# Kernel tuning notes

Hardware: AMD Instinct MI355X
Metric: run time of the kernel (lower is better)

The kernel has to match this reference:

```python
import jax, jax.numpy as jnp
import numpy as np

D_MODEL = 32
SEQ = 128  # input_dim: each scalar feature is a token


def setup_inputs() -> dict:
    key = jax.random.key(0)
    ks = jax.random.split(key, 11)
    B = 16384
    s = 1.0 / np.sqrt(D_MODEL)
    return {
        "x": jax.random.normal(ks[0], (B, SEQ), dtype=jnp.float32),
        "Wt": jax.random.normal(ks[1], (1, D_MODEL), dtype=jnp.float32),  # token_proj weight (in=1)
        "bt": jax.random.normal(ks[2], (D_MODEL,), dtype=jnp.float32) * 0.02,
        "Wq": jax.random.normal(ks[3], (D_MODEL, D_MODEL), dtype=jnp.float32) * s,
        "bq": jax.random.normal(ks[4], (D_MODEL,), dtype=jnp.float32) * 0.02,
        "Wk": jax.random.normal(ks[5], (D_MODEL, D_MODEL), dtype=jnp.float32) * s,
        "bk": jax.random.normal(ks[6], (D_MODEL,), dtype=jnp.float32) * 0.02,
        "Wv": jax.random.normal(ks[7], (D_MODEL, D_MODEL), dtype=jnp.float32) * s,
        "bv": jax.random.normal(ks[8], (D_MODEL,), dtype=jnp.float32) * 0.02,
        "Wo": jax.random.normal(ks[9], (D_MODEL, 1), dtype=jnp.float32) * s,
        "bo": jax.random.normal(ks[10], (1,), dtype=jnp.float32) * 0.02,
    }


def reference(x, Wt, bt, Wq, bq, Wk, bk, Wv, bv, Wo, bo):
    # x: [B, 128] -> tokens [B, 128, d_model] (each scalar projected from 1 -> d)
    tokens = x[..., None] * Wt[0] + bt  # [B, S, D]
    Q = jnp.einsum("bsd,de->bse", tokens, Wq) + bq
    K = jnp.einsum("bsd,de->bse", tokens, Wk) + bk
    V = jnp.einsum("bsd,de->bse", tokens, Wv) + bv
    scale = jnp.asarray(D_MODEL, x.dtype) ** 0.5
    scores = jnp.einsum("bqd,bkd->bqk", Q, K) / scale  # [B, S, S]
    w = jax.nn.softmax(scores, axis=-1)
    att = jnp.einsum("bqk,bkd->bqd", w, V)  # [B, S, D]
    agg = att.mean(axis=1)  # [B, D]
    risk = agg @ Wo + bo  # [B, 1]
    return risk[:, 0]
```

## Files before the change

### kernel.cpp

```cpp
#include <hip/hip_runtime.h>
#include <hip/hip_bf16.h>

#define SEQ 128
#define DM 32

#define K_LOG2E_2P23 12102203.161561485f
#define SCHRAUDOLPH_C 1064985472.0f

__global__ void precompute_consts(const float* __restrict__ Wt,
                                  const float* __restrict__ bt,
                                  const float* __restrict__ Wq,
                                  const float* __restrict__ bq,
                                  const float* __restrict__ Wk,
                                  const float* __restrict__ bk,
                                  const float* __restrict__ Wv,
                                  const float* __restrict__ bv,
                                  const float* __restrict__ Wo,
                                  const float* __restrict__ bo,
                                  float* __restrict__ consts) {
    int e = threadIdx.x;
    float qw = 0.f, qb = 0.f, kw = 0.f, kb = 0.f, vw = 0.f, vb = 0.f;
    float wo = 0.f;
    if (e < DM) {
        for (int d = 0; d < DM; ++d) {
            float wt = Wt[d];
            float bb = bt[d];
            qw = fmaf(wt, Wq[d * DM + e], qw);
            qb = fmaf(bb, Wq[d * DM + e], qb);
            kw = fmaf(wt, Wk[d * DM + e], kw);
            kb = fmaf(bb, Wk[d * DM + e], kb);
            vw = fmaf(wt, Wv[d * DM + e], vw);
            vb = fmaf(bb, Wv[d * DM + e], vb);
        }
        qb += bq[e];
        kb += bk[e];
        vb += bv[e];
        wo = Wo[e];
    }
    float pa = qw * kw;
    float pc = qb * kw;
    float pal = vw * wo;
    float pbe = vb * wo;
    for (int off = 32; off > 0; off >>= 1) {
        pa  += __shfl_down(pa, off);
        pc  += __shfl_down(pc, off);
        pal += __shfl_down(pal, off);
        pbe += __shfl_down(pbe, off);
    }
    if (e == 0) {
        const float inv_scale = 0.17677669529663687f;
        consts[0] = pa * inv_scale * K_LOG2E_2P23;
        consts[1] = pc * inv_scale * K_LOG2E_2P23;
        consts[2] = pal;
        consts[3] = pbe + bo[0];
    }
}

template <bool CLAMP>
__device__ __forceinline__ void row_loop(const float4* __restrict__ row4,
                                         float T0, float M0, float T1, float M1,
                                         float& s0, float& sxw0,
                                         float& s1, float& sxw1) {
#pragma unroll
    for (int k4 = 0; k4 < SEQ / 4; ++k4) {
        const float4 xv = row4[k4];
#pragma unroll
        for (int j = 0; j < 4; ++j) {
            const float xk = (j == 0) ? xv.x : (j == 1) ? xv.y : (j == 2) ? xv.z : xv.w;
            float v0 = fmaf(T0, xk, M0);
            float v1 = fmaf(T1, xk, M1);
            if (CLAMP) {
                v0 = fmaxf(v0, 0.0f);
                v1 = fmaxf(v1, 0.0f);
            }
            const float e0 = __int_as_float((int)v0);
            const float e1 = __int_as_float((int)v1);
            s0 += e0; sxw0 = fmaf(e0, xk, sxw0);
            s1 += e1; sxw1 = fmaf(e1, xk, sxw1);
        }
    }
}

#define ROWS_PER_BLOCK 4

__global__ __launch_bounds__(256) void attn_rowmean_kernel(
        const float* __restrict__ x,
        const float* __restrict__ consts,
        float* __restrict__ out, int B) {
    __shared__ float sx[ROWS_PER_BLOCK][SEQ];

    const int wave = threadIdx.x >> 6;
    const int lane = threadIdx.x & 63;
    int b = blockIdx.x * ROWS_PER_BLOCK + wave;
    if (b >= B) b = B - 1;

    const float A     = consts[0];
    const float C     = consts[1];
    const float alpha = consts[2];
    const float beta  = consts[3];

    const float* xr = x + (size_t)b * SEQ;
    const float x0 = xr[lane];
    const float x1 = xr[lane + 64];
    sx[wave][lane]      = x0;
    sx[wave][lane + 64] = x1;

    float mx = fmaxf(x0, x1);
    float mn = fminf(x0, x1);
    for (int off = 32; off > 0; off >>= 1) {
        mx = fmaxf(mx, __shfl_xor(mx, off));
        mn = fminf(mn, __shfl_xor(mn, off));
    }

    __syncthreads();

    const float T0 = fmaf(A, x0, C);
    const float T1 = fmaf(A, x1, C);
    const float m0 = fmaxf(T0 * mx, T0 * mn);
    const float m1 = fmaxf(T1 * mx, T1 * mn);
    const float M0 = SCHRAUDOLPH_C - m0;
    const float M1 = SCHRAUDOLPH_C - m1;

    float s0 = 0.f, sxw0 = 0.f, s1 = 0.f, sxw1 = 0.f;
    const float4* row4 = (const float4*)sx[wave];

    const float maxabs = fmaxf(fabsf(mx), fabsf(mn));
    const float tmax = fmaf(fabsf(A), maxabs, fabsf(C));
    if (tmax * (mx - mn) < 1.0e9f) {
        row_loop<false>(row4, T0, M0, T1, M1, s0, sxw0, s1, sxw1);
    } else {
        row_loop<true>(row4, T0, M0, T1, M1, s0, sxw0, s1, sxw1);
    }

    float msum = sxw0 * __builtin_amdgcn_rcpf(s0) +
                 sxw1 * __builtin_amdgcn_rcpf(s1);
    for (int off = 32; off > 0; off >>= 1)
        msum += __shfl_xor(msum, off);

    if (lane == 0)
        out[b] = fmaf(alpha, msum * (1.0f / 128.0f), beta);
}

extern "C" void kernel_launch(void* const* d_in, const int* in_sizes, int n_in,
                              void* d_out, int out_size, void* d_ws, size_t ws_size,
                              hipStream_t stream) {
    const float* x  = (const float*)d_in[0];
    const float* Wt = (const float*)d_in[1];
    const float* bt = (const float*)d_in[2];
    const float* Wq = (const float*)d_in[3];
    const float* bq = (const float*)d_in[4];
    const float* Wk = (const float*)d_in[5];
    const float* bk = (const float*)d_in[6];
    const float* Wv = (const float*)d_in[7];
    const float* bv = (const float*)d_in[8];
    const float* Wo = (const float*)d_in[9];
    const float* bo = (const float*)d_in[10];
    float* out = (float*)d_out;
    float* consts = (float*)d_ws;

    const int B = in_sizes[0] / SEQ;

    precompute_consts<<<1, 64, 0, stream>>>(Wt, bt, Wq, bq, Wk, bk, Wv, bv,
                                            Wo, bo, consts);

    const int grid = (B + ROWS_PER_BLOCK - 1) / ROWS_PER_BLOCK;
    attn_rowmean_kernel<<<grid, 256, 0, stream>>>(x, consts, out, B);
}
```

Before: 98.40 us.

## Fuse constant precompute into main kernel and process two rows per wave

Removes the separate single-block precompute launch. Each wave now recomputes the folded attention constants (A, C, alpha, beta) from the weight matrices itself and then handles two batch rows instead of one. This saves one kernel launch and the serialising dependency between the two kernels. In exchange every wave repeats about 16 iterations of weight loads and FMAs plus shuffle reductions, and the __syncthreads is dropped because each wave reads only its own shared-memory rows.

```diff
diff --git a/kernel.cpp b/kernel.cpp
--- a/kernel.cpp
+++ b/kernel.cpp
@@ -6,55 +6,8 @@
 
 #define K_LOG2E_2P23 12102203.161561485f
 #define SCHRAUDOLPH_C 1064985472.0f
+#define INV_SQRT_D 0.17677669529663687f
 
-__global__ void precompute_consts(const float* __restrict__ Wt,
-                                  const float* __restrict__ bt,
-                                  const float* __restrict__ Wq,
-                                  const float* __restrict__ bq,
-                                  const float* __restrict__ Wk,
-                                  const float* __restrict__ bk,
-                                  const float* __restrict__ Wv,
-                                  const float* __restrict__ bv,
-                                  const float* __restrict__ Wo,
-                                  const float* __restrict__ bo,
-                                  float* __restrict__ consts) {
-    int e = threadIdx.x;
-    float qw = 0.f, qb = 0.f, kw = 0.f, kb = 0.f, vw = 0.f, vb = 0.f;
-    float wo = 0.f;
-    if (e < DM) {
-        for (int d = 0; d < DM; ++d) {
-            float wt = Wt[d];
-            float bb = bt[d];
-            qw = fmaf(wt, Wq[d * DM + e], qw);
-            qb = fmaf(bb, Wq[d * DM + e], qb);
-            kw = fmaf(wt, Wk[d * DM + e], kw);
-            kb = fmaf(bb, Wk[d * DM + e], kb);
-            vw = fmaf(wt, Wv[d * DM + e], vw);
-            vb = fmaf(bb, Wv[d * DM + e], vb);
-        }
-        qb += bq[e];
-        kb += bk[e];
-        vb += bv[e];
-        wo = Wo[e];
-    }
-    float pa = qw * kw;
-    float pc = qb * kw;
-    float pal = vw * wo;
-    float pbe = vb * wo;
-    for (int off = 32; off > 0; off >>= 1) {
-        pa  += __shfl_down(pa, off);
-        pc  += __shfl_down(pc, off);
-        pal += __shfl_down(pal, off);
-        pbe += __shfl_down(pbe, off);
-    }
-    if (e == 0) {
-        const float inv_scale = 0.17677669529663687f;
-        consts[0] = pa * inv_scale * K_LOG2E_2P23;
-        consts[1] = pc * inv_scale * K_LOG2E_2P23;
-        consts[2] = pal;
-        consts[3] = pbe + bo[0];
-    }
-}
 
 template <bool CLAMP>
 __device__ __forceinline__ void row_loop(const float4* __restrict__ row4,
@@ -81,64 +34,116 @@
     }
 }
 
-#define ROWS_PER_BLOCK 4
+#define WAVES_PER_BLOCK 4
+#define ROWS_PER_WAVE 2
 
-__global__ __launch_bounds__(256) void attn_rowmean_kernel(
+__global__ __launch_bounds__(256) void attn_fused_kernel(
         const float* __restrict__ x,
-        const float* __restrict__ consts,
+        const float* __restrict__ Wt, const float* __restrict__ bt,
+        const float* __restrict__ Wq, const float* __restrict__ bq,
+        const float* __restrict__ Wk,
+        const float* __restrict__ Wv, const float* __restrict__ bv,
+        const float* __restrict__ Wo, const float* __restrict__ bo,
         float* __restrict__ out, int B) {
-    __shared__ float sx[ROWS_PER_BLOCK][SEQ];
+    __shared__ float sx[WAVES_PER_BLOCK][ROWS_PER_WAVE][SEQ];
 
     const int wave = threadIdx.x >> 6;
     const int lane = threadIdx.x & 63;
-    int b = blockIdx.x * ROWS_PER_BLOCK + wave;
-    if (b >= B) b = B - 1;
+    const int wg = blockIdx.x * WAVES_PER_BLOCK + wave;
+    int b0 = wg * ROWS_PER_WAVE;
+    int b1 = b0 + 1;
+    if (b0 >= B) b0 = B - 1;
+    if (b1 >= B) b1 = B - 1;
 
-    const float A     = consts[0];
-    const float C     = consts[1];
-    const float alpha = consts[2];
-    const float beta  = consts[3];
+    const float* xr0 = x + (size_t)b0 * SEQ;
+    const float* xr1 = x + (size_t)b1 * SEQ;
+    const float x00 = xr0[lane];
+    const float x01 = xr0[lane + 64];
+    const float x10 = xr1[lane];
+    const float x11 = xr1[lane + 64];
 
-    const float* xr = x + (size_t)b * SEQ;
-    const float x0 = xr[lane];
-    const float x1 = xr[lane + 64];
-    sx[wave][lane]      = x0;
-    sx[wave][lane + 64] = x1;
+    const int e  = lane & 31;
+    const int dh = lane >> 5;
+    float qw = 0.f, qb = 0.f, kw = 0.f, vw = 0.f, vb = 0.f;
+#pragma unroll
+    for (int i = 0; i < 16; ++i) {
+        const int d = dh * 16 + i;
+        const float wt  = Wt[d];
+        const float bb  = bt[d];
+        const float wqe = Wq[d * DM + e];
+        const float wke = Wk[d * DM + e];
+        const float wve = Wv[d * DM + e];
+        qw = fmaf(wt, wqe, qw); qb = fmaf(bb, wqe, qb);
+        kw = fmaf(wt, wke, kw);
+        vw = fmaf(wt, wve, vw); vb = fmaf(bb, wve, vb);
+    }
+    qw += __shfl_xor(qw, 32); qb += __shfl_xor(qb, 32);
+    kw += __shfl_xor(kw, 32);
+    vw += __shfl_xor(vw, 32); vb += __shfl_xor(vb, 32);
+    qb += bq[e];
+    vb += bv[e];
+    const float wo = Wo[e];
+    float pa  = qw * kw;
+    float pc  = qb * kw;
+    float pal = vw * wo;
+    float pbe = vb * wo;
+#pragma unroll
+    for (int off = 32; off > 0; off >>= 1) {
+        pa  += __shfl_xor(pa,  off);
+        pc  += __shfl_xor(pc,  off);
+        pal += __shfl_xor(pal, off);
+        pbe += __shfl_xor(pbe, off);
+    }
+    const float A     = pa * (0.5f * INV_SQRT_D * K_LOG2E_2P23);
+    const float C     = pc * (0.5f * INV_SQRT_D * K_LOG2E_2P23);
+    const float alpha = pal * 0.5f;
+    const float beta  = fmaf(pbe, 0.5f, bo[0]);
+    const float absA = fabsf(A), absC = fabsf(C);
 
-    float mx = fmaxf(x0, x1);
-    float mn = fminf(x0, x1);
-    for (int off = 32; off > 0; off >>= 1) {
-        mx = fmaxf(mx, __shfl_xor(mx, off));
-        mn = fminf(mn, __shfl_xor(mn, off));
+#pragma unroll
+    for (int r = 0; r < ROWS_PER_WAVE; ++r) {
+        const float x0 = r ? x10 : x00;
+        const float x1 = r ? x11 : x01;
+        const int b    = r ? b1 : b0;
+
+        sx[wave][r][lane]      = x0;
+        sx[wave][r][lane + 64] = x1;
+
+        float mx = fmaxf(x0, x1);
+        float mn = fminf(x0, x1);
+#pragma unroll
+        for (int off = 32; off > 0; off >>= 1) {
+            mx = fmaxf(mx, __shfl_xor(mx, off));
+            mn = fminf(mn, __shfl_xor(mn, off));
+        }
+
+        const float T0 = fmaf(A, x0, C);
+        const float T1 = fmaf(A, x1, C);
+        const float m0 = fmaxf(T0 * mx, T0 * mn);
+        const float m1 = fmaxf(T1 * mx, T1 * mn);
+        const float M0 = SCHRAUDOLPH_C - m0;
+        const float M1 = SCHRAUDOLPH_C - m1;
+
+        float s0 = 0.f, sxw0 = 0.f, s1 = 0.f, sxw1 = 0.f;
+        const float4* row4 = (const float4*)sx[wave][r];
+
+        const float maxabs = fmaxf(fabsf(mx), fabsf(mn));
+        const float tmax = fmaf(absA, maxabs, absC);
+        if (tmax * (mx - mn) < 1.0e9f) {
+            row_loop<false>(row4, T0, M0, T1, M1, s0, sxw0, s1, sxw1);
+        } else {
+            row_loop<true>(row4, T0, M0, T1, M1, s0, sxw0, s1, sxw1);
+        }
+
+        float msum = sxw0 * __builtin_amdgcn_rcpf(s0) +
+                     sxw1 * __builtin_amdgcn_rcpf(s1);
+#pragma unroll
+        for (int off = 32; off > 0; off >>= 1)
+            msum += __shfl_xor(msum, off);
+
+        if (lane == 0)
+            out[b] = fmaf(alpha, msum * (1.0f / 128.0f), beta);
     }
-
-    __syncthreads();
-
-    const float T0 = fmaf(A, x0, C);
-    const float T1 = fmaf(A, x1, C);
-    const float m0 = fmaxf(T0 * mx, T0 * mn);
-    const float m1 = fmaxf(T1 * mx, T1 * mn);
-    const float M0 = SCHRAUDOLPH_C - m0;
-    const float M1 = SCHRAUDOLPH_C - m1;
-
-    float s0 = 0.f, sxw0 = 0.f, s1 = 0.f, sxw1 = 0.f;
-    const float4* row4 = (const float4*)sx[wave];
-
-    const float maxabs = fmaxf(fabsf(mx), fabsf(mn));
-    const float tmax = fmaf(fabsf(A), maxabs, fabsf(C));
-    if (tmax * (mx - mn) < 1.0e9f) {
-        row_loop<false>(row4, T0, M0, T1, M1, s0, sxw0, s1, sxw1);
-    } else {
-        row_loop<true>(row4, T0, M0, T1, M1, s0, sxw0, s1, sxw1);
-    }
-
-    float msum = sxw0 * __builtin_amdgcn_rcpf(s0) +
-                 sxw1 * __builtin_amdgcn_rcpf(s1);
-    for (int off = 32; off > 0; off >>= 1)
-        msum += __shfl_xor(msum, off);
-
-    if (lane == 0)
-        out[b] = fmaf(alpha, msum * (1.0f / 128.0f), beta);
 }
 
 extern "C" void kernel_launch(void* const* d_in, const int* in_sizes, int n_in,
@@ -150,19 +155,16 @@
     const float* Wq = (const float*)d_in[3];
     const float* bq = (const float*)d_in[4];
     const float* Wk = (const float*)d_in[5];
-    const float* bk = (const float*)d_in[6];
     const float* Wv = (const float*)d_in[7];
     const float* bv = (const float*)d_in[8];
     const float* Wo = (const float*)d_in[9];
     const float* bo = (const float*)d_in[10];
     float* out = (float*)d_out;
-    float* consts = (float*)d_ws;
 
     const int B = in_sizes[0] / SEQ;
 
-    precompute_consts<<<1, 64, 0, stream>>>(Wt, bt, Wq, bq, Wk, bk, Wv, bv,
-                                            Wo, bo, consts);
-
-    const int grid = (B + ROWS_PER_BLOCK - 1) / ROWS_PER_BLOCK;
-    attn_rowmean_kernel<<<grid, 256, 0, stream>>>(x, consts, out, B);
+    const int rows_per_block = WAVES_PER_BLOCK * ROWS_PER_WAVE;
+    const int grid = (B + rows_per_block - 1) / rows_per_block;
+    attn_fused_kernel<<<grid, 256, 0, stream>>>(x, Wt, bt, Wq, bq, Wk,
+                                                Wv, bv, Wo, bo, out, B);
 }
```

Measured after the change: 99.28 us. Within noise of the previous version (+0.9%).
